# Performance work log

Hardware: AMD Instinct MI355X
Metric: run time of the kernel (lower is better)

The kernel has to match this reference:

```python
import jax, jax.numpy as jnp
import numpy as np

TOP_K = 8
THRESHOLD = 0.0        # similarity_threshold
SELF_SIM = 0.999       # exclude_self cutoff
EPS = 1e-12            # F.normalize eps


def _l2_normalize(x):
    # matches torch.nn.functional.normalize(p=2, dim=-1, eps=1e-12)
    n = jnp.linalg.norm(x, axis=-1, keepdims=True)
    return x / jnp.maximum(n, EPS)


def setup_inputs() -> dict:
    key = jax.random.key(0)
    kq, km = jax.random.split(key)
    B, N, D = 2048, 65536, 512
    q = jax.random.normal(kq, (B, D), dtype=jnp.float32)
    mem = jax.random.normal(km, (N, D), dtype=jnp.float32)
    # add_memories() stores L2-normalized representations when normalize=True
    mem = _l2_normalize(mem)
    return {"query_representations": q, "memory_bank": mem}


def reference(query_representations, memory_bank):
    # normalize queries (config.normalize_memories=True)
    q = _l2_normalize(query_representations)            # [B, D]
    # cosine similarity: bank rows already unit-norm
    sims = jnp.einsum("bd,nd->bn", q, memory_bank)      # [B, N]
    neg_inf = jnp.float32(-jnp.inf)
    # exclude_self: mask near-exact matches
    sims = jnp.where(sims > SELF_SIM, neg_inf, sims)
    # threshold mask
    sims = jnp.where(sims >= THRESHOLD, sims, neg_inf)
    # top-k (k = min(top_k, count) = TOP_K since bank is full)
    top_sims, top_idx = jax.lax.top_k(sims, TOP_K)      # [B, K]
    retrieved = memory_bank[top_idx]                    # [B, K, D] gather
    mask = top_sims > neg_inf                           # [B, K] valid entries
    return retrieved, top_sims, mask
```

## Files before the change

kernel.cpp:

```cpp
#include <hip/hip_runtime.h>
#include <math.h>

#define D        512
#define NQ       2048
#define NMEM     65536
#define TOPK     8
#define NCAND    32
#define SELF_SIM 0.999f
#define FSCALE   64.0f
#define TAU_RAW  483.328f
#define CAP      448
#define SCAP     768

#define QB     128
#define SPAN   1024
#define NSPL   64
#define NROUND 64
#define BUFSZ  16384u

typedef __attribute__((ext_vector_type(4))) float f32x4;
typedef __attribute__((ext_vector_type(2))) unsigned long u64x2;

__device__ __forceinline__ void gl_lds16(const void* g, void* l) {
    __builtin_amdgcn_global_load_lds(
        (const __attribute__((address_space(1))) void*)g,
        (__attribute__((address_space(3))) void*)l, 16, 0, 0);
}

__device__ __forceinline__ unsigned pack4_fp8(float4 v) {
    int lo = __builtin_amdgcn_cvt_pk_fp8_f32(v.x * FSCALE, v.y * FSCALE, 0, false);
    return (unsigned)__builtin_amdgcn_cvt_pk_fp8_f32(v.z * FSCALE, v.w * FSCALE, lo, true);
}

__global__ __launch_bounds__(256)
void k_prep(const float* __restrict__ mem, const float* __restrict__ q,
            unsigned* __restrict__ mp8, unsigned* __restrict__ qp8,
            double* __restrict__ qinv)
{
    if (blockIdx.x < 2048) {
        const int i = blockIdx.x * 256 + threadIdx.x;
        const int row = i >> 3, p = i & 7;
        const float4* pf = (const float4*)(mem + (size_t)row * D + p * 64);
        float4 f[16];
        #pragma unroll
        for (int t = 0; t < 16; ++t) f[t] = pf[t];
        const int nblk = row >> 7, t8 = (row >> 4) & 7, fc = row & 15;
        uint4* dst = (uint4*)mp8 + ((size_t)nblk * 4096 + p * 512 + t8 * 64 + fc);
        #pragma unroll
        for (int fr = 0; fr < 4; ++fr) {
            uint4 c;
            c.x = pack4_fp8(f[fr * 2]);
            c.y = pack4_fp8(f[fr * 2 + 1]);
            c.z = pack4_fp8(f[8 + fr * 2]);
            c.w = pack4_fp8(f[8 + fr * 2 + 1]);
            dst[fr * 16] = c;
        }
    } else {
        __shared__ float rb[4][512];
        const int wv = threadIdx.x >> 6, lane = threadIdx.x & 63;
        const int row = (blockIdx.x - 2048) * 4 + wv;
        const float4* src = (const float4*)(q + (size_t)row * D);
        float4 v0 = src[lane];
        float4 v1 = src[lane + 64];
        double ss = (double)v0.x*v0.x + (double)v0.y*v0.y + (double)v0.z*v0.z + (double)v0.w*v0.w
                  + (double)v1.x*v1.x + (double)v1.y*v1.y + (double)v1.z*v1.z + (double)v1.w*v1.w;
        #pragma unroll
        for (int off = 32; off >= 1; off >>= 1)
            ss += __shfl_xor(ss, off, 64);
        double inv = 1.0 / fmax(sqrt(ss), 1e-12);
        float invf = (float)inv;
        ((float4*)rb[wv])[lane]      = make_float4(v0.x*invf, v0.y*invf, v0.z*invf, v0.w*invf);
        ((float4*)rb[wv])[lane + 64] = make_float4(v1.x*invf, v1.y*invf, v1.z*invf, v1.w*invf);
        if (lane == 0) qinv[row] = inv;
        __syncthreads();
        if (lane < 32) {
            const int p = lane >> 2, fr = lane & 3;
            const float* f = rb[wv] + p * 64 + fr * 8;
            uint4 c;
            c.x = pack4_fp8(*(const float4*)(f));
            c.y = pack4_fp8(*(const float4*)(f + 4));
            c.z = pack4_fp8(*(const float4*)(f + 32));
            c.w = pack4_fp8(*(const float4*)(f + 36));
            const int qblk = row >> 8, qb16 = (row >> 4) & 15, fc = row & 15;
            ((uint4*)qp8)[(size_t)qblk * 8192 + p * 1024 + qb16 * 64 + fr * 16 + fc] = c;
        }
    }
}

__global__ __launch_bounds__(256, 4)
void k_cand(const char* __restrict__ qp8, const char* __restrict__ mp8,
            unsigned* __restrict__ cnt, uint2* __restrict__ cbuf)
{
    __shared__ __align__(16) char smem[32768 + 16 + SCAP * 8];
    unsigned* scnt = (unsigned*)(smem + 32768);
    uint2*    sbuf = (uint2*)   (smem + 32784);

    const int tid = threadIdx.x;
    const int w = tid >> 6, l = tid & 63;
    const int fc = l & 15, fr = l >> 4;

    const int id  = blockIdx.x;
    const int xcd = id & 7;
    const int j   = id >> 3;
    const int qblk = j & 15;
    const int sg   = j >> 4;
    const int split = xcd + 8 * sg;
    const int qbase = qblk * QB;
    const int nbase = split * SPAN;

    const unsigned qpanel = (unsigned)(qblk >> 1) * 131072u + (unsigned)(qblk & 1) * 8192u;
    const unsigned mpanel = (unsigned)(nbase >> 7) * 65536u;
    const unsigned dc0 = (unsigned)tid * 16u;
    const unsigned dc1 = dc0 + 4096u;

    if (tid == 0) *scnt = 0u;

    f32x4 acc[2][8];
    const int lofs = l * 16;

#define STAGE(R, B)                                                            \
    {   const unsigned r_ = (unsigned)(R);                                     \
        const unsigned p_ = r_ & 7u;                                           \
        const unsigned qoff = qpanel + p_ * 16384u;                            \
        const unsigned moff = mpanel + (r_ >> 3) * 65536u + p_ * 8192u;        \
        gl_lds16(qp8 + qoff + dc0, smem + (B) + dc0);                          \
        gl_lds16(qp8 + qoff + dc1, smem + (B) + dc1);                          \
        gl_lds16(mp8 + moff + dc0, smem + (B) + 8192u + dc0);                  \
        gl_lds16(mp8 + moff + dc1, smem + (B) + 8192u + dc1);                  \
    }

    unsigned cb = 0u;
    STAGE(0, cb);

    for (int r = 0; r < NROUND; ++r) {
        const int kp = r & 7, sub = r >> 3;
        if (kp == 0) {
            #pragma unroll
            for (int jj = 0; jj < 2; ++jj)
                #pragma unroll
                for (int t = 0; t < 8; ++t) acc[jj][t] = (f32x4){0.f, 0.f, 0.f, 0.f};
        }
        asm volatile("" ::: "memory");
        __builtin_amdgcn_s_barrier();
        asm volatile("" ::: "memory");
        if (r + 1 < NROUND) {
            STAGE(r + 1, cb ^ BUFSZ);
            asm volatile("s_waitcnt vmcnt(4)" ::: "memory");
        } else {
            asm volatile("s_waitcnt vmcnt(0)" ::: "memory");
        }
        __builtin_amdgcn_s_barrier();
        asm volatile("" ::: "memory");

        {
            const char* Qs = smem + cb;
            const char* Ms = smem + cb + 8192;
            u64x2 qf0 = *(const u64x2*)(Qs + (2 * w) * 1024 + lofs);
            u64x2 qf1 = *(const u64x2*)(Qs + (2 * w + 1) * 1024 + lofs);
            __builtin_amdgcn_s_setprio(1);
            #pragma unroll
            for (int t = 0; t < 8; ++t) {
                u64x2 a = *(const u64x2*)(Ms + t * 1024 + lofs);
                acc[0][t] = __builtin_amdgcn_mfma_f32_16x16x32_fp8_fp8((long)a[0], (long)qf0[0], acc[0][t], 0, 0, 0);
                acc[1][t] = __builtin_amdgcn_mfma_f32_16x16x32_fp8_fp8((long)a[0], (long)qf1[0], acc[1][t], 0, 0, 0);
                acc[0][t] = __builtin_amdgcn_mfma_f32_16x16x32_fp8_fp8((long)a[1], (long)qf0[1], acc[0][t], 0, 0, 0);
                acc[1][t] = __builtin_amdgcn_mfma_f32_16x16x32_fp8_fp8((long)a[1], (long)qf1[1], acc[1][t], 0, 0, 0);
            }
            __builtin_amdgcn_s_setprio(0);
        }
        if (kp == 7) {
            const int nb0 = nbase + sub * 128 + fr * 4;
            #pragma unroll
            for (int jj = 0; jj < 2; ++jj) {
                float tm[8];
                #pragma unroll
                for (int t = 0; t < 8; ++t)
                    tm[t] = fmaxf(fmaxf(acc[jj][t][0], acc[jj][t][1]),
                                  fmaxf(acc[jj][t][2], acc[jj][t][3]));
                float m = tm[0];
                #pragma unroll
                for (int t = 1; t < 8; ++t) m = fmaxf(m, tm[t]);
                if (m > TAU_RAW) {
                    const unsigned qloc = (unsigned)(w * 32 + jj * 16 + fc);
                    #pragma unroll
                    for (int t = 0; t < 8; ++t) if (tm[t] > TAU_RAW) {
                        #pragma unroll
                        for (int rr = 0; rr < 4; ++rr) {
                            const float v = acc[jj][t][rr];
                            if (v > TAU_RAW) {
                                unsigned p = atomicAdd(scnt, 1u);
                                if (p < SCAP)
                                    sbuf[p] = make_uint2(__float_as_uint(v),
                                        (qloc << 16) | (unsigned)(nb0 + t * 16 + rr));
                            }
                        }
                    }
                }
            }
        }
        cb ^= BUFSZ;
    }
#undef STAGE

    __syncthreads();
    const unsigned ns = min(*scnt, (unsigned)SCAP);
    for (unsigned i = tid; i < ns; i += 256) {
        const uint2 e = sbuf[i];
        const int qg = qbase + (int)(e.y >> 16);
        const unsigned p = atomicAdd(&cnt[qg], 1u);
        if (p < CAP)
            cbuf[(size_t)qg * CAP + p] = make_uint2(e.x, e.y & 0xffffu);
    }
}

__global__ __launch_bounds__(256)
void k_final(const unsigned* __restrict__ cnt, const uint2* __restrict__ cbuf,
             const float* __restrict__ q, const float* __restrict__ mem,
             const double* __restrict__ qinv, float* __restrict__ out)
{
    __shared__ unsigned long long keys[CAP];
    __shared__ int    scand[NCAND];
    __shared__ double rsv[NCAND];
    __shared__ int    fidx[TOPK];

    const int qq  = blockIdx.x;
    const int tid = threadIdx.x;
    const int n = (int)min(cnt[qq], (unsigned)CAP);

    if (tid < NCAND) scand[tid] = -1;
    const uint2* src = cbuf + (size_t)qq * CAP;
    for (int c = tid; c < n; c += 256) {
        const uint2 e = src[c];
        keys[c] = ((unsigned long long)e.x << 16)
                | (unsigned long long)(0xffffu - (e.y & 0xffffu));
    }
    __syncthreads();
    for (int c = tid; c < n; c += 256) {
        const unsigned long long my = keys[c];
        int rank = 0;
        for (int j2 = 0; j2 < n; ++j2) rank += (keys[j2] > my) ? 1 : 0;
        if (rank < NCAND) scand[rank] = 0xffff - (int)(my & 0xffffu);
    }
    __syncthreads();

    const int w = tid >> 6, lane = tid & 63;
    float qv[8];
    #pragma unroll
    for (int t = 0; t < 8; ++t) qv[t] = q[(size_t)qq * D + t * 64 + lane];
    for (int ci = w * 8; ci < w * 8 + 8; ++ci) {
        const int m = scand[ci];
        double s = 0.0;
        if (m >= 0) {
            const float* mp = mem + (size_t)m * D;
            #pragma unroll
            for (int t = 0; t < 8; ++t)
                s += (double)qv[t] * (double)mp[t * 64 + lane];
        }
        #pragma unroll
        for (int off = 32; off >= 1; off >>= 1)
            s += __shfl_xor(s, off, 64);
        if (lane == 0) rsv[ci] = (m >= 0) ? s * qinv[qq] : -1.0 / 0.0;
    }
    __syncthreads();

    if (tid < NCAND) {
        double x = rsv[tid];
        if (scand[tid] < 0 || x > (double)SELF_SIM || x < 0.0) x = -1.0 / 0.0;
        rsv[tid] = x;
    }
    __syncthreads();
    if (tid < NCAND) {
        const double x  = rsv[tid];
        const int    mi = (scand[tid] < 0) ? 0x7fffffff : scand[tid];
        int rank = 0;
        for (int j2 = 0; j2 < NCAND; ++j2) {
            const double xj = rsv[j2];
            const int    ij = (scand[j2] < 0) ? 0x7fffffff : scand[j2];
            if (xj > x || (xj == x && (ij < mi || (ij == mi && j2 < tid)))) ++rank;
        }
        if (rank < TOPK) {
            float* tops  = out + (size_t)NQ * TOPK * D;
            float* maskp = tops + (size_t)NQ * TOPK;
            tops [qq * TOPK + rank] = (float)x;
            maskp[qq * TOPK + rank] = (x == -INFINITY) ? 0.0f : 1.0f;
            fidx [rank] = (scand[tid] < 0) ? 0 : scand[tid];
        }
    }
    __syncthreads();

    for (int i = tid; i < TOPK * (D / 4); i += 256) {
        const int s2 = i >> 7;
        const int d4 = i & 127;
        const int sr = fidx[s2];
        ((float4*)out)[((size_t)qq * TOPK + s2) * (D / 4) + d4] =
            ((const float4*)mem)[(size_t)sr * (D / 4) + d4];
    }
}

extern "C" void kernel_launch(void* const* d_in, const int* in_sizes, int n_in,
                              void* d_out, int out_size, void* d_ws, size_t ws_size,
                              hipStream_t stream)
{
    const float* q   = (const float*)d_in[0];
    const float* mem = (const float*)d_in[1];
    float* out = (float*)d_out;
    char* ws = (char*)d_ws;

    unsigned* mp8  = (unsigned*)(ws);
    unsigned* qp8  = (unsigned*)(ws + ((size_t)32 << 20));
    unsigned* cnt  = (unsigned*)(ws + ((size_t)33 << 20));
    uint2*    cbuf = (uint2*)   (ws + ((size_t)34 << 20));
    double*   qinv = (double*)  (ws + ((size_t)42 << 20));

    hipMemsetAsync(cnt, 0, NQ * sizeof(unsigned), stream);

    k_prep<<<2560, 256, 0, stream>>>(mem, q, mp8, qp8, qinv);
    k_cand<<<(NQ / QB) * NSPL, 256, 0, stream>>>((const char*)qp8, (const char*)mp8, cnt, cbuf);
    k_final<<<NQ, 256, 0, stream>>>(cnt, cbuf, q, mem, qinv, out);
}
```

Baseline: 207.5 us.

## Switch candidate GEMM to 16x16x128 scaled FP8 MFMA with smaller query tiles

Replaces the 16x16x32 fp8 MFMA with the MI355X 16x16x128 f8f6f4 scaled MFMA, which handles four times the K depth per instruction. The fp8 packing layout of both the memory bank and the queries is reorganised to match the new operand layout. Query tiles shrink from 128 to 64 rows and query fragments are now loaded straight from global memory into registers, so LDS holds only bank tiles. This doubles the block count and halves rounds per block, at the cost of more redundant bank reads and a smaller local candidate buffer.

Result: slower. 226.5 us (+9.1%).

```diff
diff --git a/kernel.cpp b/kernel.cpp
--- a/kernel.cpp
+++ b/kernel.cpp
@@ -10,16 +10,16 @@
 #define FSCALE   64.0f
 #define TAU_RAW  483.328f
 #define CAP      448
-#define SCAP     768
-
-#define QB     128
+#define SCAP     512
+
+#define QB     64
 #define SPAN   1024
-#define NSPL   64
-#define NROUND 64
+#define NROUND 32
 #define BUFSZ  16384u
 
 typedef __attribute__((ext_vector_type(4))) float f32x4;
-typedef __attribute__((ext_vector_type(2))) unsigned long u64x2;
+typedef __attribute__((ext_vector_type(4))) int   i32x4;
+typedef __attribute__((ext_vector_type(8))) int   i32x8;
 
 __device__ __forceinline__ void gl_lds16(const void* g, void* l) {
     __builtin_amdgcn_global_load_lds(
@@ -45,16 +45,19 @@
         #pragma unroll
         for (int t = 0; t < 16; ++t) f[t] = pf[t];
         const int nblk = row >> 7, t8 = (row >> 4) & 7, fc = row & 15;
-        uint4* dst = (uint4*)mp8 + ((size_t)nblk * 4096 + p * 512 + t8 * 64 + fc);
+        const int kq = p >> 1, fb = (p & 1) * 2;
+        uint4* dst = (uint4*)mp8 + ((size_t)nblk * 4096 + kq * 1024 + t8 * 128);
         #pragma unroll
-        for (int fr = 0; fr < 4; ++fr) {
-            uint4 c;
-            c.x = pack4_fp8(f[fr * 2]);
-            c.y = pack4_fp8(f[fr * 2 + 1]);
-            c.z = pack4_fp8(f[8 + fr * 2]);
-            c.w = pack4_fp8(f[8 + fr * 2 + 1]);
-            dst[fr * 16] = c;
-        }
+        for (int u = 0; u < 2; ++u)
+            #pragma unroll
+            for (int h = 0; h < 2; ++h) {
+                uint4 c;
+                c.x = pack4_fp8(f[u * 8 + h * 4 + 0]);
+                c.y = pack4_fp8(f[u * 8 + h * 4 + 1]);
+                c.z = pack4_fp8(f[u * 8 + h * 4 + 2]);
+                c.w = pack4_fp8(f[u * 8 + h * 4 + 3]);
+                dst[h * 64 + (fb + u) * 16 + fc] = c;
+            }
     } else {
         __shared__ float rb[4][512];
         const int wv = threadIdx.x >> 6, lane = threadIdx.x & 63;
@@ -74,15 +77,15 @@
         if (lane == 0) qinv[row] = inv;
         __syncthreads();
         if (lane < 32) {
-            const int p = lane >> 2, fr = lane & 3;
-            const float* f = rb[wv] + p * 64 + fr * 8;
+            const int kq = lane >> 3, fr = (lane >> 1) & 3, h = lane & 1;
+            const float* f = rb[wv] + kq * 128 + fr * 32 + h * 16;
             uint4 c;
             c.x = pack4_fp8(*(const float4*)(f));
             c.y = pack4_fp8(*(const float4*)(f + 4));
-            c.z = pack4_fp8(*(const float4*)(f + 32));
-            c.w = pack4_fp8(*(const float4*)(f + 36));
-            const int qblk = row >> 8, qb16 = (row >> 4) & 15, fc = row & 15;
-            ((uint4*)qp8)[(size_t)qblk * 8192 + p * 1024 + qb16 * 64 + fr * 16 + fc] = c;
+            c.z = pack4_fp8(*(const float4*)(f + 8));
+            c.w = pack4_fp8(*(const float4*)(f + 12));
+            const int qblk = row >> 6, t4 = (row >> 4) & 3, fc = row & 15;
+            ((uint4*)qp8)[(size_t)qblk * 2048 + kq * 512 + t4 * 128 + h * 64 + fr * 16 + fc] = c;
         }
     }
 }
@@ -102,97 +105,87 @@
     const int id  = blockIdx.x;
     const int xcd = id & 7;
     const int j   = id >> 3;
-    const int qblk = j & 15;
-    const int sg   = j >> 4;
+    const int qblk = j & 31;
+    const int sg   = j >> 5;
     const int split = xcd + 8 * sg;
     const int qbase = qblk * QB;
     const int nbase = split * SPAN;
 
-    const unsigned qpanel = (unsigned)(qblk >> 1) * 131072u + (unsigned)(qblk & 1) * 8192u;
+    const char* qpan = qp8 + (size_t)qblk * 32768u + (unsigned)w * 2048u + (unsigned)l * 16u;
     const unsigned mpanel = (unsigned)(nbase >> 7) * 65536u;
-    const unsigned dc0 = (unsigned)tid * 16u;
-    const unsigned dc1 = dc0 + 4096u;
 
     if (tid == 0) *scnt = 0u;
 
-    f32x4 acc[2][8];
+    f32x4 acc[8];
     const int lofs = l * 16;
 
 #define STAGE(R, B)                                                            \
     {   const unsigned r_ = (unsigned)(R);                                     \
-        const unsigned p_ = r_ & 7u;                                           \
-        const unsigned qoff = qpanel + p_ * 16384u;                            \
-        const unsigned moff = mpanel + (r_ >> 3) * 65536u + p_ * 8192u;        \
-        gl_lds16(qp8 + qoff + dc0, smem + (B) + dc0);                          \
-        gl_lds16(qp8 + qoff + dc1, smem + (B) + dc1);                          \
-        gl_lds16(mp8 + moff + dc0, smem + (B) + 8192u + dc0);                  \
-        gl_lds16(mp8 + moff + dc1, smem + (B) + 8192u + dc1);                  \
+        const unsigned base_ = mpanel + (r_ >> 2) * 65536u + (r_ & 3u) * 16384u; \
+        gl_lds16(mp8 + base_ + (unsigned)tid * 16u,          smem + (B) + (unsigned)tid * 16u); \
+        gl_lds16(mp8 + base_ + (unsigned)tid * 16u + 4096u,  smem + (B) + (unsigned)tid * 16u + 4096u); \
+        gl_lds16(mp8 + base_ + (unsigned)tid * 16u + 8192u,  smem + (B) + (unsigned)tid * 16u + 8192u); \
+        gl_lds16(mp8 + base_ + (unsigned)tid * 16u + 12288u, smem + (B) + (unsigned)tid * 16u + 12288u); \
     }
 
     unsigned cb = 0u;
     STAGE(0, cb);
 
     for (int r = 0; r < NROUND; ++r) {
-        const int kp = r & 7, sub = r >> 3;
-        if (kp == 0) {
-            #pragma unroll
-            for (int jj = 0; jj < 2; ++jj)
-                #pragma unroll
-                for (int t = 0; t < 8; ++t) acc[jj][t] = (f32x4){0.f, 0.f, 0.f, 0.f};
+        const int kq = r & 3, sub = r >> 2;
+        if (kq == 0) {
+            #pragma unroll
+            for (int t = 0; t < 8; ++t) acc[t] = (f32x4){0.f, 0.f, 0.f, 0.f};
         }
         asm volatile("" ::: "memory");
         __builtin_amdgcn_s_barrier();
         asm volatile("" ::: "memory");
+        i32x4 q0, q1;
+        {
+            const char* qa = qpan + (unsigned)kq * 8192u;
+            asm volatile("global_load_dwordx4 %0, %1, off"             : "=v"(q0) : "v"(qa) : "memory");
+            asm volatile("global_load_dwordx4 %0, %1, off offset:1024" : "=v"(q1) : "v"(qa) : "memory");
+        }
         if (r + 1 < NROUND) {
             STAGE(r + 1, cb ^ BUFSZ);
             asm volatile("s_waitcnt vmcnt(4)" ::: "memory");
         } else {
             asm volatile("s_waitcnt vmcnt(0)" ::: "memory");
         }
+        __builtin_amdgcn_sched_barrier(0);
         __builtin_amdgcn_s_barrier();
         asm volatile("" ::: "memory");
 
         {
-            const char* Qs = smem + cb;
-            const char* Ms = smem + cb + 8192;
-            u64x2 qf0 = *(const u64x2*)(Qs + (2 * w) * 1024 + lofs);
-            u64x2 qf1 = *(const u64x2*)(Qs + (2 * w + 1) * 1024 + lofs);
+            const char* Ms = smem + cb;
+            const i32x8 bv = __builtin_shufflevector(q0, q1, 0, 1, 2, 3, 4, 5, 6, 7);
             __builtin_amdgcn_s_setprio(1);
             #pragma unroll
             for (int t = 0; t < 8; ++t) {
-                u64x2 a = *(const u64x2*)(Ms + t * 1024 + lofs);
-                acc[0][t] = __builtin_amdgcn_mfma_f32_16x16x32_fp8_fp8((long)a[0], (long)qf0[0], acc[0][t], 0, 0, 0);
-                acc[1][t] = __builtin_amdgcn_mfma_f32_16x16x32_fp8_fp8((long)a[0], (long)qf1[0], acc[1][t], 0, 0, 0);
-                acc[0][t] = __builtin_amdgcn_mfma_f32_16x16x32_fp8_fp8((long)a[1], (long)qf0[1], acc[0][t], 0, 0, 0);
-                acc[1][t] = __builtin_amdgcn_mfma_f32_16x16x32_fp8_fp8((long)a[1], (long)qf1[1], acc[1][t], 0, 0, 0);
+                i32x4 lo = *(const i32x4*)(Ms + t * 2048 + lofs);
+                i32x4 hi = *(const i32x4*)(Ms + t * 2048 + 1024 + lofs);
+                i32x8 av = __builtin_shufflevector(lo, hi, 0, 1, 2, 3, 4, 5, 6, 7);
+                acc[t] = __builtin_amdgcn_mfma_scale_f32_16x16x128_f8f6f4(
+                            av, bv, acc[t], 0, 0, 0, 0x7F7F7F7F, 0, 0x7F7F7F7F);
             }
             __builtin_amdgcn_s_setprio(0);
         }
-        if (kp == 7) {
+        if (kq == 3) {
             const int nb0 = nbase + sub * 128 + fr * 4;
-            #pragma unroll
-            for (int jj = 0; jj < 2; ++jj) {
-                float tm[8];
-                #pragma unroll
-                for (int t = 0; t < 8; ++t)
-                    tm[t] = fmaxf(fmaxf(acc[jj][t][0], acc[jj][t][1]),
-                                  fmaxf(acc[jj][t][2], acc[jj][t][3]));
-                float m = tm[0];
-                #pragma unroll
-                for (int t = 1; t < 8; ++t) m = fmaxf(m, tm[t]);
-                if (m > TAU_RAW) {
-                    const unsigned qloc = (unsigned)(w * 32 + jj * 16 + fc);
+            const unsigned qloc = (unsigned)(w * 16 + fc);
+            #pragma unroll
+            for (int t = 0; t < 8; ++t) {
+                const float tm = fmaxf(fmaxf(acc[t][0], acc[t][1]),
+                                       fmaxf(acc[t][2], acc[t][3]));
+                if (tm > TAU_RAW) {
                     #pragma unroll
-                    for (int t = 0; t < 8; ++t) if (tm[t] > TAU_RAW) {
-                        #pragma unroll
-                        for (int rr = 0; rr < 4; ++rr) {
-                            const float v = acc[jj][t][rr];
-                            if (v > TAU_RAW) {
-                                unsigned p = atomicAdd(scnt, 1u);
-                                if (p < SCAP)
-                                    sbuf[p] = make_uint2(__float_as_uint(v),
-                                        (qloc << 16) | (unsigned)(nb0 + t * 16 + rr));
-                            }
+                    for (int rr = 0; rr < 4; ++rr) {
+                        const float v = acc[t][rr];
+                        if (v > TAU_RAW) {
+                            unsigned p = atomicAdd(scnt, 1u);
+                            if (p < SCAP)
+                                sbuf[p] = make_uint2(__float_as_uint(v),
+                                    (qloc << 16) | (unsigned)(nb0 + t * 16 + rr));
                         }
                     }
                 }
@@ -315,6 +308,6 @@
     hipMemsetAsync(cnt, 0, NQ * sizeof(unsigned), stream);
 
     k_prep<<<2560, 256, 0, stream>>>(mem, q, mp8, qp8, qinv);
-    k_cand<<<(NQ / QB) * NSPL, 256, 0, stream>>>((const char*)qp8, (const char*)mp8, cnt, cbuf);
+    k_cand<<<(NQ / QB) * (NMEM / SPAN), 256, 0, stream>>>((const char*)qp8, (const char*)mp8, cnt, cbuf);
     k_final<<<NQ, 256, 0, stream>>>(cnt, cbuf, q, mem, qinv, out);
 }
```
